# Performance work log

Hardware: AMD Instinct MI355X
Metric: run time of the kernel (lower is better)

## Reference

```python
import jax, jax.numpy as jnp
import numpy as np

N = 8192  # num_nodes
E = 8192  # num_edges (== N so self-loops sit on the diagonal)
C = 256   # in_channels
ALPHA = 0.1
BETA = 0.5


def setup_inputs() -> dict:
    key = jax.random.key(0)
    k1, k2, k3 = jax.random.split(key, 3)
    x_0 = jax.random.normal(k1, (N, C), dtype=jnp.float32)
    # binary hypergraph incidence with self-loops on the diagonal
    mask = (jax.random.uniform(k2, (N, E)) < 0.004).astype(jnp.float32)
    idx = jnp.arange(N)
    incidence_1 = mask.at[idx, idx].set(1.0)
    # torch Linear(C, C, bias=False) weight, Kaiming-uniform-ish scale
    W = jax.random.normal(k3, (C, C), dtype=jnp.float32) / jnp.sqrt(C)
    return {"x_0": x_0, "incidence_1": incidence_1, "W": W}


def reference(x_0, incidence_1, W):
    # 1) edge aggregation: m_{0->1} = B^T x  -> [E, C]
    m_0_1 = incidence_1.T @ x_0
    # degree normalization (matches diag/to_dense math without materializing diag)
    node_degree = jnp.sum(incidence_1, axis=1)                      # [N]
    edge_degree = (node_degree @ incidence_1) / jnp.sum(incidence_1, axis=0)  # [E]
    # 2) node aggregation with 1/sqrt(d_z), 1/sqrt(d_x) scaling
    m_1_0 = (incidence_1 @ (m_0_1 / jnp.sqrt(edge_degree)[:, None])) \
            / jnp.sqrt(node_degree)[:, None]                        # [N, C]
    # 3) skip + learned update (x_skip defaults to x_0)
    x_combined = (1.0 - ALPHA) * m_1_0 + ALPHA * x_0
    return (1.0 - BETA) * x_combined + BETA * (x_combined @ W.T)
```

## Files before the change

### kernel.cpp

```cpp
#include <hip/hip_runtime.h>
#include <hip/hip_bf16.h>

#define NN 8192
#define NE 8192
#define CC 256
#define CAP 128

typedef __attribute__((ext_vector_type(8))) short bf16x8;
typedef __attribute__((ext_vector_type(8))) unsigned short u16x8;
typedef __attribute__((ext_vector_type(4))) float f32x4;

static __device__ __forceinline__ ushort f2b(float f) {
    unsigned u = __float_as_uint(f);
    return (ushort)((u + 0x7fffu + ((u >> 16) & 1u)) >> 16);
}
static __device__ __forceinline__ float b2f(ushort u) {
    return __uint_as_float((unsigned)u << 16);
}

__global__ __launch_bounds__(256) void k1_scan(const float* __restrict__ B,
                                               const float* __restrict__ x0,
                                               const float* __restrict__ W,
                                               ushort* __restrict__ x0b,
                                               ushort* __restrict__ Wb,
                                               int* __restrict__ csr,
                                               int* __restrict__ row_cnt,
                                               int* __restrict__ col_cnt,
                                               int* __restrict__ csc,
                                               float* __restrict__ edge_wsum) {
    __shared__ int wcnt[4];
    {
        int i = blockIdx.x * 1024 + threadIdx.x * 4;
        float4 v = *(const float4*)(x0 + i);
        ushort4 u; u.x = f2b(v.x); u.y = f2b(v.y); u.z = f2b(v.z); u.w = f2b(v.w);
        *(ushort4*)(x0b + i) = u;
        if (blockIdx.x < 64) {
            float4 w = *(const float4*)(W + i);
            ushort4 uw; uw.x = f2b(w.x); uw.y = f2b(w.y); uw.z = f2b(w.z); uw.w = f2b(w.w);
            *(ushort4*)(Wb + i) = uw;
        }
    }
    const int wave = threadIdx.x >> 6;
    const int lane = threadIdx.x & 63;
    const int row  = blockIdx.x * 4 + wave;
    const float4* rp = (const float4*)(B + (size_t)row * NE);
    int* outp = csr + (size_t)row * CAP;
    if (lane == 0) wcnt[wave] = 0;
    float4 v = rp[lane];
    #pragma unroll 1
    for (int it = 0; it < 32; ++it) {
        float4 vn = v;
        if (it < 31) vn = rp[(it + 1) * 64 + lane];
        float fs = v.x + v.y + v.z + v.w;
        if (__ballot(fs != 0.f)) {
            int m = (int)fs;
            int pos = 0;
            if (m) pos = atomicAdd(&wcnt[wave], m);
            int e0 = (it * 64 + lane) * 4;
            if (v.x != 0.f) { if (pos < CAP) outp[pos] = e0;     ++pos; }
            if (v.y != 0.f) { if (pos < CAP) outp[pos] = e0 + 1; ++pos; }
            if (v.z != 0.f) { if (pos < CAP) outp[pos] = e0 + 2; ++pos; }
            if (v.w != 0.f) { if (pos < CAP) outp[pos] = e0 + 3; ++pos; }
        }
        v = vn;
    }
    int cnt = wcnt[wave];
    cnt = cnt < CAP ? cnt : CAP;
    if (lane == 0) row_cnt[row] = cnt;
    const float deg = (float)cnt;
    for (int i = lane; i < cnt; i += 64) {
        int e = outp[i];
        int pos = atomicAdd(&col_cnt[e], 1);
        if (pos < CAP) csc[(size_t)e * CAP + pos] = row;
        atomicAdd(&edge_wsum[e], deg);
    }
}

__global__ __launch_bounds__(256) void k4_edge_agg(const ushort* __restrict__ x0b,
                                                   const int* __restrict__ csc,
                                                   const int* __restrict__ col_cnt,
                                                   const float* __restrict__ edge_wsum,
                                                   ushort* __restrict__ m01s) {
    const int wave = threadIdx.x >> 6;
    const int lane = threadIdx.x & 63;
    const int half = lane >> 5;
    const int cl = lane & 31;
    const int e = blockIdx.x * 4 + wave;
    int cnt = col_cnt[e]; if (cnt > CAP) cnt = CAP;
    const float er = rsqrtf(edge_wsum[e] / (float)cnt);
    const int* cp = csc + (size_t)e * CAP;
    const int idx = cp[lane];
    const ushort* xb = x0b + cl * 8;
    float a0[8] = {}, a1[8] = {};
    const int lim = cnt < 64 ? cnt : 64;
    int i = 0;
    for (; i + 8 <= lim; i += 8) {
        int n0 = __shfl(idx, i + half);
        int n1 = __shfl(idx, i + 2 + half);
        int n2 = __shfl(idx, i + 4 + half);
        int n3 = __shfl(idx, i + 6 + half);
        u16x8 r0 = *(const u16x8*)(xb + (size_t)n0 * CC);
        u16x8 r1 = *(const u16x8*)(xb + (size_t)n1 * CC);
        u16x8 r2 = *(const u16x8*)(xb + (size_t)n2 * CC);
        u16x8 r3 = *(const u16x8*)(xb + (size_t)n3 * CC);
        #pragma unroll
        for (int c = 0; c < 8; ++c) {
            a0[c] += b2f(r0[c]); a1[c] += b2f(r1[c]);
            a0[c] += b2f(r2[c]); a1[c] += b2f(r3[c]);
        }
    }
    for (; i + 2 <= lim; i += 2) {
        int n0 = __shfl(idx, i + half);
        u16x8 r0 = *(const u16x8*)(xb + (size_t)n0 * CC);
        #pragma unroll
        for (int c = 0; c < 8; ++c) a0[c] += b2f(r0[c]);
    }
    if (i < lim) {
        int n0 = __shfl(idx, i);
        if (half == 0) {
            u16x8 r0 = *(const u16x8*)(xb + (size_t)n0 * CC);
            #pragma unroll
            for (int c = 0; c < 8; ++c) a0[c] += b2f(r0[c]);
        }
    }
    if (cnt > 64 && half == 0) {
        for (int j = 64; j < cnt; ++j) {
            int n2 = cp[j];
            u16x8 r0 = *(const u16x8*)(xb + (size_t)n2 * CC);
            #pragma unroll
            for (int c = 0; c < 8; ++c) a0[c] += b2f(r0[c]);
        }
    }
    u16x8 r8;
    #pragma unroll
    for (int c = 0; c < 8; ++c) {
        float t = a0[c] + a1[c];
        t += __shfl_xor(t, 32);
        r8[c] = f2b(t * er);
    }
    if (half == 0) *(u16x8*)(m01s + (size_t)e * CC + cl * 8) = r8;
}

__global__ __launch_bounds__(1024, 8) void k5_fused(const ushort* __restrict__ x0b,
                                                    const ushort* __restrict__ m01s,
                                                    const int* __restrict__ csr,
                                                    const int* __restrict__ row_cnt,
                                                    const ushort* __restrict__ Wb,
                                                    float* __restrict__ out) {
    __shared__ __align__(16) ushort xs[16][264];
    const int w = threadIdx.x >> 6;
    const int lane = threadIdx.x & 63;
    const int half = lane >> 5;
    const int cl = lane & 31;
    const int n = blockIdx.x * 16 + w;
    const int cnt = row_cnt[n];
    const float nr = rsqrtf((float)cnt);
    const int* ep = csr + (size_t)n * CAP;
    const int idx = ep[lane];
    const ushort* mb = m01s + cl * 8;
    float a0[8] = {}, a1[8] = {};
    const int lim = cnt < 64 ? cnt : 64;
    int i = 0;
    for (; i + 8 <= lim; i += 8) {
        int e0 = __shfl(idx, i + half);
        int e1 = __shfl(idx, i + 2 + half);
        int e2 = __shfl(idx, i + 4 + half);
        int e3 = __shfl(idx, i + 6 + half);
        u16x8 r0 = *(const u16x8*)(mb + (size_t)e0 * CC);
        u16x8 r1 = *(const u16x8*)(mb + (size_t)e1 * CC);
        u16x8 r2 = *(const u16x8*)(mb + (size_t)e2 * CC);
        u16x8 r3 = *(const u16x8*)(mb + (size_t)e3 * CC);
        #pragma unroll
        for (int c = 0; c < 8; ++c) {
            a0[c] += b2f(r0[c]); a1[c] += b2f(r1[c]);
            a0[c] += b2f(r2[c]); a1[c] += b2f(r3[c]);
        }
    }
    for (; i + 2 <= lim; i += 2) {
        int e0 = __shfl(idx, i + half);
        u16x8 r0 = *(const u16x8*)(mb + (size_t)e0 * CC);
        #pragma unroll
        for (int c = 0; c < 8; ++c) a0[c] += b2f(r0[c]);
    }
    if (i < lim) {
        int e0 = __shfl(idx, i);
        if (half == 0) {
            u16x8 r0 = *(const u16x8*)(mb + (size_t)e0 * CC);
            #pragma unroll
            for (int c = 0; c < 8; ++c) a0[c] += b2f(r0[c]);
        }
    }
    if (cnt > 64 && half == 0) {
        for (int j = 64; j < cnt; ++j) {
            int e2 = ep[j];
            u16x8 r0 = *(const u16x8*)(mb + (size_t)e2 * CC);
            #pragma unroll
            for (int c = 0; c < 8; ++c) a0[c] += b2f(r0[c]);
        }
    }
    u16x8 x = *(const u16x8*)(x0b + (size_t)n * CC + cl * 8);
    const float s = 0.9f * nr;
    u16x8 r8;
    #pragma unroll
    for (int c = 0; c < 8; ++c) {
        float t = a0[c] + a1[c];
        t += __shfl_xor(t, 32);
        r8[c] = f2b(s * t + 0.1f * b2f(x[c]));
    }
    if (half == 0) *(u16x8*)(&xs[w][cl * 8]) = r8;
    __syncthreads();
    const int lr = lane & 15, lk = lane >> 4;
    const int n0 = w * 16;
    f32x4 acc = {0.f, 0.f, 0.f, 0.f};
    #pragma unroll
    for (int kb = 0; kb < 8; ++kb) {
        bf16x8 a = *(const bf16x8*)(&xs[lr][kb * 32 + lk * 8]);
        bf16x8 b = *(const bf16x8*)(Wb + (size_t)(n0 + lr) * CC + kb * 32 + lk * 8);
        acc = __builtin_amdgcn_mfma_f32_16x16x32_bf16(a, b, acc, 0, 0, 0);
    }
    const size_t rb = (size_t)blockIdx.x * 16;
    #pragma unroll
    for (int r = 0; r < 4; ++r) {
        int row = lk * 4 + r;
        int col = n0 + lr;
        float sk = b2f(xs[row][col]);
        out[(rb + row) * CC + col] = 0.5f * sk + 0.5f * acc[r];
    }
}

extern "C" void kernel_launch(void* const* d_in, const int* in_sizes, int n_in,
                              void* d_out, int out_size, void* d_ws, size_t ws_size,
                              hipStream_t stream) {
    const float* x0 = (const float*)d_in[0];
    const float* B  = (const float*)d_in[1];
    const float* W  = (const float*)d_in[2];
    float* out = (float*)d_out;

    char* ws = (char*)d_ws;
    const size_t need = (17ull << 20) + 4ull * NE * 4;
    if (ws_size < need) return;

    int*    csr       = (int*)(ws);
    int*    csc       = (int*)(ws + (4ull << 20));
    ushort* m01s      = (ushort*)(ws + (8ull << 20));
    ushort* x0b       = (ushort*)(ws + (12ull << 20));
    ushort* Wb        = (ushort*)(ws + (16ull << 20));
    int*    row_cnt   = (int*)(ws + (16ull << 20) + (256u << 10));
    int*    col_cnt   = row_cnt + NN;
    float*  edge_wsum = (float*)(col_cnt + NE);

    hipMemsetAsync(col_cnt, 0, 2ull * NE * 4, stream);

    k1_scan<<<NN / 4, 256, 0, stream>>>(B, x0, W, x0b, Wb, csr, row_cnt, col_cnt, csc, edge_wsum);
    k4_edge_agg<<<NE / 4, 256, 0, stream>>>(x0b, csc, col_cnt, edge_wsum, m01s);
    k5_fused<<<NN / 16, 1024, 0, stream>>>(x0b, m01s, csr, row_cnt, Wb, out);
}
```

Before: 103.8 us.

## Split gathers into channel slabs and unfuse dense GEMM into separate kernel

The edge and node aggregation kernels now split the 256 channels into two 128-channel slabs handled by separate blocks, with four row-groups per wave gathering neighbors in parallel. This doubles the block count and changes the memory access granularity. The node kernel no longer does the W GEMM in place. It writes the combined bf16 activations to a new workspace buffer, and a new standalone MFMA GEMM kernel computes the output with four 16-column tiles per wave. This trades an extra kernel launch and a round trip of the activations through memory for better parallelism and no 1024-thread blocks with shared-memory sync.

New measurement: 111.4 us. 1.07x slower.

```diff
diff --git a/kernel.cpp b/kernel.cpp
--- a/kernel.cpp
+++ b/kernel.cpp
@@ -76,155 +76,167 @@
     }
 }
 
-__global__ __launch_bounds__(256) void k4_edge_agg(const ushort* __restrict__ x0b,
-                                                   const int* __restrict__ csc,
-                                                   const int* __restrict__ col_cnt,
-                                                   const float* __restrict__ edge_wsum,
-                                                   ushort* __restrict__ m01s) {
+__global__ __launch_bounds__(256) void k4_slab(const ushort* __restrict__ x0b,
+                                               const int* __restrict__ csc,
+                                               const int* __restrict__ col_cnt,
+                                               const float* __restrict__ edge_wsum,
+                                               ushort* __restrict__ m01s) {
     const int wave = threadIdx.x >> 6;
     const int lane = threadIdx.x & 63;
-    const int half = lane >> 5;
-    const int cl = lane & 31;
-    const int e = blockIdx.x * 4 + wave;
+    const int g = lane >> 4;
+    const int c = lane & 15;
+    const int slab = blockIdx.x & 1;
+    const int e = (blockIdx.x >> 1) * 4 + wave;
     int cnt = col_cnt[e]; if (cnt > CAP) cnt = CAP;
     const float er = rsqrtf(edge_wsum[e] / (float)cnt);
     const int* cp = csc + (size_t)e * CAP;
     const int idx = cp[lane];
-    const ushort* xb = x0b + cl * 8;
+    const ushort* xb = x0b + slab * 128 + c * 8;
     float a0[8] = {}, a1[8] = {};
     const int lim = cnt < 64 ? cnt : 64;
     int i = 0;
     for (; i + 8 <= lim; i += 8) {
-        int n0 = __shfl(idx, i + half);
-        int n1 = __shfl(idx, i + 2 + half);
-        int n2 = __shfl(idx, i + 4 + half);
-        int n3 = __shfl(idx, i + 6 + half);
-        u16x8 r0 = *(const u16x8*)(xb + (size_t)n0 * CC);
-        u16x8 r1 = *(const u16x8*)(xb + (size_t)n1 * CC);
-        u16x8 r2 = *(const u16x8*)(xb + (size_t)n2 * CC);
-        u16x8 r3 = *(const u16x8*)(xb + (size_t)n3 * CC);
-        #pragma unroll
-        for (int c = 0; c < 8; ++c) {
-            a0[c] += b2f(r0[c]); a1[c] += b2f(r1[c]);
-            a0[c] += b2f(r2[c]); a1[c] += b2f(r3[c]);
-        }
-    }
-    for (; i + 2 <= lim; i += 2) {
-        int n0 = __shfl(idx, i + half);
-        u16x8 r0 = *(const u16x8*)(xb + (size_t)n0 * CC);
-        #pragma unroll
-        for (int c = 0; c < 8; ++c) a0[c] += b2f(r0[c]);
-    }
-    if (i < lim) {
-        int n0 = __shfl(idx, i);
-        if (half == 0) {
-            u16x8 r0 = *(const u16x8*)(xb + (size_t)n0 * CC);
+        int na = __shfl(idx, i + g);
+        int nb = __shfl(idx, i + 4 + g);
+        u16x8 ra = *(const u16x8*)(xb + (size_t)na * CC);
+        u16x8 rb = *(const u16x8*)(xb + (size_t)nb * CC);
+        #pragma unroll
+        for (int k = 0; k < 8; ++k) { a0[k] += b2f(ra[k]); a1[k] += b2f(rb[k]); }
+    }
+    if (i + 4 <= lim) {
+        int na = __shfl(idx, i + g);
+        u16x8 ra = *(const u16x8*)(xb + (size_t)na * CC);
+        #pragma unroll
+        for (int k = 0; k < 8; ++k) a0[k] += b2f(ra[k]);
+        i += 4;
+    }
+    {
+        int na = __shfl(idx, (i + g) & 63);
+        if (i + g < lim) {
+            u16x8 ra = *(const u16x8*)(xb + (size_t)na * CC);
             #pragma unroll
-            for (int c = 0; c < 8; ++c) a0[c] += b2f(r0[c]);
-        }
-    }
-    if (cnt > 64 && half == 0) {
+            for (int k = 0; k < 8; ++k) a0[k] += b2f(ra[k]);
+        }
+    }
+    if (cnt > 64) {
         for (int j = 64; j < cnt; ++j) {
             int n2 = cp[j];
-            u16x8 r0 = *(const u16x8*)(xb + (size_t)n2 * CC);
-            #pragma unroll
-            for (int c = 0; c < 8; ++c) a0[c] += b2f(r0[c]);
+            if (g == 0) {
+                u16x8 ra = *(const u16x8*)(xb + (size_t)n2 * CC);
+                #pragma unroll
+                for (int k = 0; k < 8; ++k) a0[k] += b2f(ra[k]);
+            }
         }
     }
     u16x8 r8;
     #pragma unroll
-    for (int c = 0; c < 8; ++c) {
-        float t = a0[c] + a1[c];
+    for (int k = 0; k < 8; ++k) {
+        float t = a0[k] + a1[k];
+        t += __shfl_xor(t, 16);
         t += __shfl_xor(t, 32);
-        r8[c] = f2b(t * er);
-    }
-    if (half == 0) *(u16x8*)(m01s + (size_t)e * CC + cl * 8) = r8;
-}
-
-__global__ __launch_bounds__(1024, 8) void k5_fused(const ushort* __restrict__ x0b,
-                                                    const ushort* __restrict__ m01s,
-                                                    const int* __restrict__ csr,
-                                                    const int* __restrict__ row_cnt,
-                                                    const ushort* __restrict__ Wb,
-                                                    float* __restrict__ out) {
-    __shared__ __align__(16) ushort xs[16][264];
-    const int w = threadIdx.x >> 6;
-    const int lane = threadIdx.x & 63;
-    const int half = lane >> 5;
-    const int cl = lane & 31;
-    const int n = blockIdx.x * 16 + w;
+        r8[k] = f2b(t * er);
+    }
+    if (g == 0) *(u16x8*)(m01s + (size_t)e * CC + slab * 128 + c * 8) = r8;
+}
+
+__global__ __launch_bounds__(256) void k5_slab(const ushort* __restrict__ x0b,
+                                               const ushort* __restrict__ m01s,
+                                               const int* __restrict__ csr,
+                                               const int* __restrict__ row_cnt,
+                                               ushort* __restrict__ xcb) {
+    const int wave = threadIdx.x >> 6;
+    const int lane = threadIdx.x & 63;
+    const int g = lane >> 4;
+    const int c = lane & 15;
+    const int slab = blockIdx.x & 1;
+    const int n = (blockIdx.x >> 1) * 4 + wave;
     const int cnt = row_cnt[n];
     const float nr = rsqrtf((float)cnt);
     const int* ep = csr + (size_t)n * CAP;
     const int idx = ep[lane];
-    const ushort* mb = m01s + cl * 8;
+    const ushort* mb = m01s + slab * 128 + c * 8;
     float a0[8] = {}, a1[8] = {};
     const int lim = cnt < 64 ? cnt : 64;
     int i = 0;
     for (; i + 8 <= lim; i += 8) {
-        int e0 = __shfl(idx, i + half);
-        int e1 = __shfl(idx, i + 2 + half);
-        int e2 = __shfl(idx, i + 4 + half);
-        int e3 = __shfl(idx, i + 6 + half);
-        u16x8 r0 = *(const u16x8*)(mb + (size_t)e0 * CC);
-        u16x8 r1 = *(const u16x8*)(mb + (size_t)e1 * CC);
-        u16x8 r2 = *(const u16x8*)(mb + (size_t)e2 * CC);
-        u16x8 r3 = *(const u16x8*)(mb + (size_t)e3 * CC);
-        #pragma unroll
-        for (int c = 0; c < 8; ++c) {
-            a0[c] += b2f(r0[c]); a1[c] += b2f(r1[c]);
-            a0[c] += b2f(r2[c]); a1[c] += b2f(r3[c]);
-        }
-    }
-    for (; i + 2 <= lim; i += 2) {
-        int e0 = __shfl(idx, i + half);
-        u16x8 r0 = *(const u16x8*)(mb + (size_t)e0 * CC);
-        #pragma unroll
-        for (int c = 0; c < 8; ++c) a0[c] += b2f(r0[c]);
-    }
-    if (i < lim) {
-        int e0 = __shfl(idx, i);
-        if (half == 0) {
-            u16x8 r0 = *(const u16x8*)(mb + (size_t)e0 * CC);
+        int ea = __shfl(idx, i + g);
+        int eb = __shfl(idx, i + 4 + g);
+        u16x8 ra = *(const u16x8*)(mb + (size_t)ea * CC);
+        u16x8 rb = *(const u16x8*)(mb + (size_t)eb * CC);
+        #pragma unroll
+        for (int k = 0; k < 8; ++k) { a0[k] += b2f(ra[k]); a1[k] += b2f(rb[k]); }
+    }
+    if (i + 4 <= lim) {
+        int ea = __shfl(idx, i + g);
+        u16x8 ra = *(const u16x8*)(mb + (size_t)ea * CC);
+        #pragma unroll
+        for (int k = 0; k < 8; ++k) a0[k] += b2f(ra[k]);
+        i += 4;
+    }
+    {
+        int ea = __shfl(idx, (i + g) & 63);
+        if (i + g < lim) {
+            u16x8 ra = *(const u16x8*)(mb + (size_t)ea * CC);
             #pragma unroll
-            for (int c = 0; c < 8; ++c) a0[c] += b2f(r0[c]);
-        }
-    }
-    if (cnt > 64 && half == 0) {
+            for (int k = 0; k < 8; ++k) a0[k] += b2f(ra[k]);
+        }
+    }
+    if (cnt > 64) {
         for (int j = 64; j < cnt; ++j) {
             int e2 = ep[j];
-            u16x8 r0 = *(const u16x8*)(mb + (size_t)e2 * CC);
-            #pragma unroll
-            for (int c = 0; c < 8; ++c) a0[c] += b2f(r0[c]);
-        }
-    }
-    u16x8 x = *(const u16x8*)(x0b + (size_t)n * CC + cl * 8);
-    const float s = 0.9f * nr;
-    u16x8 r8;
-    #pragma unroll
-    for (int c = 0; c < 8; ++c) {
-        float t = a0[c] + a1[c];
-        t += __shfl_xor(t, 32);
-        r8[c] = f2b(s * t + 0.1f * b2f(x[c]));
-    }
-    if (half == 0) *(u16x8*)(&xs[w][cl * 8]) = r8;
-    __syncthreads();
+            if (g == 0) {
+                u16x8 ra = *(const u16x8*)(mb + (size_t)e2 * CC);
+                #pragma unroll
+                for (int k = 0; k < 8; ++k) a0[k] += b2f(ra[k]);
+            }
+        }
+    }
+    float t[8];
+    #pragma unroll
+    for (int k = 0; k < 8; ++k) {
+        float s = a0[k] + a1[k];
+        s += __shfl_xor(s, 16);
+        s += __shfl_xor(s, 32);
+        t[k] = s;
+    }
+    if (g == 0) {
+        u16x8 x = *(const u16x8*)(x0b + (size_t)n * CC + slab * 128 + c * 8);
+        const float s = 0.9f * nr;
+        u16x8 r8;
+        #pragma unroll
+        for (int k = 0; k < 8; ++k) r8[k] = f2b(s * t[k] + 0.1f * b2f(x[k]));
+        *(u16x8*)(xcb + (size_t)n * CC + slab * 128 + c * 8) = r8;
+    }
+}
+
+__global__ __launch_bounds__(256) void k6_gemm(const ushort* __restrict__ xcb,
+                                               const ushort* __restrict__ Wb,
+                                               float* __restrict__ out) {
+    const int lane = threadIdx.x & 63;
+    const int gw = blockIdx.x * 4 + (threadIdx.x >> 6);
+    const int m0 = (gw >> 2) * 16;
+    const int n0 = (gw & 3) * 64;
     const int lr = lane & 15, lk = lane >> 4;
-    const int n0 = w * 16;
-    f32x4 acc = {0.f, 0.f, 0.f, 0.f};
+    f32x4 acc[4] = {};
+    const ushort* ap = xcb + (size_t)(m0 + lr) * CC + lk * 8;
     #pragma unroll
     for (int kb = 0; kb < 8; ++kb) {
-        bf16x8 a = *(const bf16x8*)(&xs[lr][kb * 32 + lk * 8]);
-        bf16x8 b = *(const bf16x8*)(Wb + (size_t)(n0 + lr) * CC + kb * 32 + lk * 8);
-        acc = __builtin_amdgcn_mfma_f32_16x16x32_bf16(a, b, acc, 0, 0, 0);
-    }
-    const size_t rb = (size_t)blockIdx.x * 16;
-    #pragma unroll
-    for (int r = 0; r < 4; ++r) {
-        int row = lk * 4 + r;
-        int col = n0 + lr;
-        float sk = b2f(xs[row][col]);
-        out[(rb + row) * CC + col] = 0.5f * sk + 0.5f * acc[r];
+        bf16x8 a = *(const bf16x8*)(ap + kb * 32);
+        #pragma unroll
+        for (int j = 0; j < 4; ++j) {
+            bf16x8 b = *(const bf16x8*)(Wb + (size_t)(n0 + j * 16 + lr) * CC + kb * 32 + lk * 8);
+            acc[j] = __builtin_amdgcn_mfma_f32_16x16x32_bf16(a, b, acc[j], 0, 0, 0);
+        }
+    }
+    #pragma unroll
+    for (int j = 0; j < 4; ++j) {
+        #pragma unroll
+        for (int r = 0; r < 4; ++r) {
+            int row = m0 + lk * 4 + r;
+            int col = n0 + j * 16 + lr;
+            float sk = b2f(xcb[(size_t)row * CC + col]);
+            out[(size_t)row * CC + col] = 0.5f * sk + 0.5f * acc[j][r];
+        }
     }
 }
 
@@ -237,21 +249,23 @@
     float* out = (float*)d_out;
 
     char* ws = (char*)d_ws;
-    const size_t need = (17ull << 20) + 4ull * NE * 4;
+    const size_t need = (21ull << 20) + 4ull * NE * 4;
     if (ws_size < need) return;
 
     int*    csr       = (int*)(ws);
     int*    csc       = (int*)(ws + (4ull << 20));
     ushort* m01s      = (ushort*)(ws + (8ull << 20));
-    ushort* x0b       = (ushort*)(ws + (12ull << 20));
-    ushort* Wb        = (ushort*)(ws + (16ull << 20));
-    int*    row_cnt   = (int*)(ws + (16ull << 20) + (256u << 10));
+    ushort* xcb       = (ushort*)(ws + (12ull << 20));
+    ushort* x0b       = (ushort*)(ws + (16ull << 20));
+    ushort* Wb        = (ushort*)(ws + (20ull << 20));
+    int*    row_cnt   = (int*)(ws + (20ull << 20) + (256u << 10));
     int*    col_cnt   = row_cnt + NN;
     float*  edge_wsum = (float*)(col_cnt + NE);
 
     hipMemsetAsync(col_cnt, 0, 2ull * NE * 4, stream);
 
     k1_scan<<<NN / 4, 256, 0, stream>>>(B, x0, W, x0b, Wb, csr, row_cnt, col_cnt, csc, edge_wsum);
-    k4_edge_agg<<<NE / 4, 256, 0, stream>>>(x0b, csc, col_cnt, edge_wsum, m01s);
-    k5_fused<<<NN / 16, 1024, 0, stream>>>(x0b, m01s, csr, row_cnt, Wb, out);
-}
+    k4_slab<<<NE / 4 * 2, 256, 0, stream>>>(x0b, csc, col_cnt, edge_wsum, m01s);
+    k5_slab<<<NN / 4 * 2, 256, 0, stream>>>(x0b, m01s, csr, row_cnt, xcb);
+    k6_gemm<<<NN * CC / 16 / 64 / 4, 256, 0, stream>>>(xcb, Wb, out);
+}
```

## Fuse scan, edge aggregation and node update into one cooperative persistent kernel

Applied to the files above, without the earlier changes.

Replaces the memset and three separate launches with one cooperative kernel of 256 blocks of 1024 threads, using grid-wide syncs between the phases: CSR scan, CSC/atomic build, edge aggregation, and node aggregation plus MFMA. The col_cnt/edge_wsum zeroing moves inside the kernel and the scan phase loses its software prefetch. The aim is to remove launch gaps and the memset. In exchange, each block covers 32 rows per phase with only 256 blocks and one block per CU, which lowers occupancy for the bandwidth-bound scan of the 256 MB incidence matrix and adds the cost of the grid syncs.

Result: slower. 211.4 us (+103.7%).

```diff
diff --git a/kernel.cpp b/kernel.cpp
--- a/kernel.cpp
+++ b/kernel.cpp
@@ -1,10 +1,15 @@
 #include <hip/hip_runtime.h>
+#include <hip/hip_cooperative_groups.h>
 #include <hip/hip_bf16.h>
+
+namespace cg = cooperative_groups;
 
 #define NN 8192
 #define NE 8192
 #define CC 256
 #define CAP 128
+#define NB 256
+#define NTH 1024
 
 typedef __attribute__((ext_vector_type(8))) short bf16x8;
 typedef __attribute__((ext_vector_type(8))) unsigned short u16x8;
@@ -18,213 +23,222 @@
     return __uint_as_float((unsigned)u << 16);
 }
 
-__global__ __launch_bounds__(256) void k1_scan(const float* __restrict__ B,
-                                               const float* __restrict__ x0,
-                                               const float* __restrict__ W,
-                                               ushort* __restrict__ x0b,
-                                               ushort* __restrict__ Wb,
-                                               int* __restrict__ csr,
-                                               int* __restrict__ row_cnt,
-                                               int* __restrict__ col_cnt,
-                                               int* __restrict__ csc,
-                                               float* __restrict__ edge_wsum) {
-    __shared__ int wcnt[4];
+__global__ __launch_bounds__(NTH, 1) void fused_all(
+        const float* __restrict__ B, const float* __restrict__ x0,
+        const float* __restrict__ W,
+        ushort* __restrict__ x0b, ushort* __restrict__ Wb,
+        int* __restrict__ csr, int* __restrict__ row_cnt,
+        int* __restrict__ col_cnt, int* __restrict__ csc,
+        float* __restrict__ edge_wsum, ushort* __restrict__ m01s,
+        float* __restrict__ out) {
+    cg::grid_group grid = cg::this_grid();
+    const int tid  = threadIdx.x;
+    const int bid  = blockIdx.x;
+    const int w    = tid >> 6;
+    const int lane = tid & 63;
+    const int half = lane >> 5;
+    const int cl   = lane & 31;
+    __shared__ int wcnt[16];
+    __shared__ __align__(16) ushort xs[32][264];
+
     {
-        int i = blockIdx.x * 1024 + threadIdx.x * 4;
-        float4 v = *(const float4*)(x0 + i);
-        ushort4 u; u.x = f2b(v.x); u.y = f2b(v.y); u.z = f2b(v.z); u.w = f2b(v.w);
-        *(ushort4*)(x0b + i) = u;
-        if (blockIdx.x < 64) {
-            float4 w = *(const float4*)(W + i);
-            ushort4 uw; uw.x = f2b(w.x); uw.y = f2b(w.y); uw.z = f2b(w.z); uw.w = f2b(w.w);
-            *(ushort4*)(Wb + i) = uw;
-        }
-    }
-    const int wave = threadIdx.x >> 6;
-    const int lane = threadIdx.x & 63;
-    const int row  = blockIdx.x * 4 + wave;
-    const float4* rp = (const float4*)(B + (size_t)row * NE);
-    int* outp = csr + (size_t)row * CAP;
-    if (lane == 0) wcnt[wave] = 0;
-    float4 v = rp[lane];
-    #pragma unroll 1
-    for (int it = 0; it < 32; ++it) {
-        float4 vn = v;
-        if (it < 31) vn = rp[(it + 1) * 64 + lane];
-        float fs = v.x + v.y + v.z + v.w;
-        if (__ballot(fs != 0.f)) {
-            int m = (int)fs;
-            int pos = 0;
-            if (m) pos = atomicAdd(&wcnt[wave], m);
-            int e0 = (it * 64 + lane) * 4;
-            if (v.x != 0.f) { if (pos < CAP) outp[pos] = e0;     ++pos; }
-            if (v.y != 0.f) { if (pos < CAP) outp[pos] = e0 + 1; ++pos; }
-            if (v.z != 0.f) { if (pos < CAP) outp[pos] = e0 + 2; ++pos; }
-            if (v.w != 0.f) { if (pos < CAP) outp[pos] = e0 + 3; ++pos; }
-        }
-        v = vn;
-    }
-    int cnt = wcnt[wave];
-    cnt = cnt < CAP ? cnt : CAP;
-    if (lane == 0) row_cnt[row] = cnt;
-    const float deg = (float)cnt;
-    for (int i = lane; i < cnt; i += 64) {
-        int e = outp[i];
-        int pos = atomicAdd(&col_cnt[e], 1);
-        if (pos < CAP) csc[(size_t)e * CAP + pos] = row;
-        atomicAdd(&edge_wsum[e], deg);
-    }
-}
-
-__global__ __launch_bounds__(256) void k4_edge_agg(const ushort* __restrict__ x0b,
-                                                   const int* __restrict__ csc,
-                                                   const int* __restrict__ col_cnt,
-                                                   const float* __restrict__ edge_wsum,
-                                                   ushort* __restrict__ m01s) {
-    const int wave = threadIdx.x >> 6;
-    const int lane = threadIdx.x & 63;
-    const int half = lane >> 5;
-    const int cl = lane & 31;
-    const int e = blockIdx.x * 4 + wave;
-    int cnt = col_cnt[e]; if (cnt > CAP) cnt = CAP;
-    const float er = rsqrtf(edge_wsum[e] / (float)cnt);
-    const int* cp = csc + (size_t)e * CAP;
-    const int idx = cp[lane];
-    const ushort* xb = x0b + cl * 8;
-    float a0[8] = {}, a1[8] = {};
-    const int lim = cnt < 64 ? cnt : 64;
-    int i = 0;
-    for (; i + 8 <= lim; i += 8) {
-        int n0 = __shfl(idx, i + half);
-        int n1 = __shfl(idx, i + 2 + half);
-        int n2 = __shfl(idx, i + 4 + half);
-        int n3 = __shfl(idx, i + 6 + half);
-        u16x8 r0 = *(const u16x8*)(xb + (size_t)n0 * CC);
-        u16x8 r1 = *(const u16x8*)(xb + (size_t)n1 * CC);
-        u16x8 r2 = *(const u16x8*)(xb + (size_t)n2 * CC);
-        u16x8 r3 = *(const u16x8*)(xb + (size_t)n3 * CC);
+        int z = bid * NTH + tid;
+        if (z < 2 * NE) col_cnt[z] = 0;
+        int i = (bid * NTH + tid) * 8;
+        f32x4 v0 = *(const f32x4*)(x0 + i);
+        f32x4 v1 = *(const f32x4*)(x0 + i + 4);
+        u16x8 u;
+        u[0]=f2b(v0.x); u[1]=f2b(v0.y); u[2]=f2b(v0.z); u[3]=f2b(v0.w);
+        u[4]=f2b(v1.x); u[5]=f2b(v1.y); u[6]=f2b(v1.z); u[7]=f2b(v1.w);
+        *(u16x8*)(x0b + i) = u;
+        if (bid < 8) {
+            f32x4 w0 = *(const f32x4*)(W + i);
+            f32x4 w1 = *(const f32x4*)(W + i + 4);
+            u16x8 uw;
+            uw[0]=f2b(w0.x); uw[1]=f2b(w0.y); uw[2]=f2b(w0.z); uw[3]=f2b(w0.w);
+            uw[4]=f2b(w1.x); uw[5]=f2b(w1.y); uw[6]=f2b(w1.z); uw[7]=f2b(w1.w);
+            *(u16x8*)(Wb + i) = uw;
+        }
+    }
+    int cnts[2];
+    #pragma unroll 1
+    for (int rr = 0; rr < 2; ++rr) {
+        const int row = bid * 32 + w * 2 + rr;
+        const f32x4* rp = (const f32x4*)(B + (size_t)row * NE);
+        int* outp = csr + (size_t)row * CAP;
+        if (lane == 0) wcnt[w] = 0;
+        #pragma unroll 1
+        for (int it = 0; it < 32; ++it) {
+            f32x4 v = rp[it * 64 + lane];
+            float fs = v.x + v.y + v.z + v.w;
+            if (__ballot(fs != 0.f)) {
+                int m = (int)fs;
+                int pos = 0;
+                if (m) pos = atomicAdd(&wcnt[w], m);
+                int e0 = (it * 64 + lane) * 4;
+                if (v.x != 0.f) { if (pos < CAP) outp[pos] = e0;     ++pos; }
+                if (v.y != 0.f) { if (pos < CAP) outp[pos] = e0 + 1; ++pos; }
+                if (v.z != 0.f) { if (pos < CAP) outp[pos] = e0 + 2; ++pos; }
+                if (v.w != 0.f) { if (pos < CAP) outp[pos] = e0 + 3; ++pos; }
+            }
+        }
+        int c = wcnt[w];
+        c = c < CAP ? c : CAP;
+        cnts[rr] = c;
+        if (lane == 0) row_cnt[row] = c;
+    }
+    grid.sync();
+    #pragma unroll 1
+    for (int rr = 0; rr < 2; ++rr) {
+        const int row = bid * 32 + w * 2 + rr;
+        const int cnt = cnts[rr];
+        const float deg = (float)cnt;
+        const int* outp = csr + (size_t)row * CAP;
+        for (int i = lane; i < cnt; i += 64) {
+            int e = outp[i];
+            int pos = atomicAdd(&col_cnt[e], 1);
+            if (pos < CAP) csc[(size_t)e * CAP + pos] = row;
+            atomicAdd(&edge_wsum[e], deg);
+        }
+    }
+    grid.sync();
+    #pragma unroll 1
+    for (int ee = 0; ee < 2; ++ee) {
+        const int e = bid * 32 + ee * 16 + w;
+        int cnt = col_cnt[e]; if (cnt > CAP) cnt = CAP;
+        const float er = rsqrtf(edge_wsum[e] / (float)cnt);
+        const int* cp = csc + (size_t)e * CAP;
+        const int idx = cp[lane];
+        const ushort* xb = x0b + cl * 8;
+        float a0[8] = {}, a1[8] = {};
+        const int lim = cnt < 64 ? cnt : 64;
+        int i = 0;
+        for (; i + 8 <= lim; i += 8) {
+            int n0 = __shfl(idx, i + half);
+            int n1 = __shfl(idx, i + 2 + half);
+            int n2 = __shfl(idx, i + 4 + half);
+            int n3 = __shfl(idx, i + 6 + half);
+            u16x8 r0 = *(const u16x8*)(xb + (size_t)n0 * CC);
+            u16x8 r1 = *(const u16x8*)(xb + (size_t)n1 * CC);
+            u16x8 r2 = *(const u16x8*)(xb + (size_t)n2 * CC);
+            u16x8 r3 = *(const u16x8*)(xb + (size_t)n3 * CC);
+            #pragma unroll
+            for (int c = 0; c < 8; ++c) {
+                a0[c] += b2f(r0[c]); a1[c] += b2f(r1[c]);
+                a0[c] += b2f(r2[c]); a1[c] += b2f(r3[c]);
+            }
+        }
+        for (; i + 2 <= lim; i += 2) {
+            int n0 = __shfl(idx, i + half);
+            u16x8 r0 = *(const u16x8*)(xb + (size_t)n0 * CC);
+            #pragma unroll
+            for (int c = 0; c < 8; ++c) a0[c] += b2f(r0[c]);
+        }
+        if (i < lim) {
+            int n0 = __shfl(idx, i);
+            if (half == 0) {
+                u16x8 r0 = *(const u16x8*)(xb + (size_t)n0 * CC);
+                #pragma unroll
+                for (int c = 0; c < 8; ++c) a0[c] += b2f(r0[c]);
+            }
+        }
+        if (cnt > 64 && half == 0) {
+            for (int j = 64; j < cnt; ++j) {
+                int n2 = cp[j];
+                u16x8 r0 = *(const u16x8*)(xb + (size_t)n2 * CC);
+                #pragma unroll
+                for (int c = 0; c < 8; ++c) a0[c] += b2f(r0[c]);
+            }
+        }
+        u16x8 r8;
         #pragma unroll
         for (int c = 0; c < 8; ++c) {
-            a0[c] += b2f(r0[c]); a1[c] += b2f(r1[c]);
-            a0[c] += b2f(r2[c]); a1[c] += b2f(r3[c]);
-        }
-    }
-    for (; i + 2 <= lim; i += 2) {
-        int n0 = __shfl(idx, i + half);
-        u16x8 r0 = *(const u16x8*)(xb + (size_t)n0 * CC);
-        #pragma unroll
-        for (int c = 0; c < 8; ++c) a0[c] += b2f(r0[c]);
-    }
-    if (i < lim) {
-        int n0 = __shfl(idx, i);
-        if (half == 0) {
-            u16x8 r0 = *(const u16x8*)(xb + (size_t)n0 * CC);
+            float t = a0[c] + a1[c];
+            t += __shfl_xor(t, 32);
+            r8[c] = f2b(t * er);
+        }
+        if (half == 0) *(u16x8*)(m01s + (size_t)e * CC + cl * 8) = r8;
+    }
+    grid.sync();
+    #pragma unroll 1
+    for (int nn2 = 0; nn2 < 2; ++nn2) {
+        const int n = bid * 32 + nn2 * 16 + w;
+        const int cnt = row_cnt[n];
+        const float nr = rsqrtf((float)cnt);
+        const int* ep = csr + (size_t)n * CAP;
+        const int idx = ep[lane];
+        const ushort* mb = m01s + cl * 8;
+        float a0[8] = {}, a1[8] = {};
+        const int lim = cnt < 64 ? cnt : 64;
+        int i = 0;
+        for (; i + 8 <= lim; i += 8) {
+            int e0 = __shfl(idx, i + half);
+            int e1 = __shfl(idx, i + 2 + half);
+            int e2 = __shfl(idx, i + 4 + half);
+            int e3 = __shfl(idx, i + 6 + half);
+            u16x8 r0 = *(const u16x8*)(mb + (size_t)e0 * CC);
+            u16x8 r1 = *(const u16x8*)(mb + (size_t)e1 * CC);
+            u16x8 r2 = *(const u16x8*)(mb + (size_t)e2 * CC);
+            u16x8 r3 = *(const u16x8*)(mb + (size_t)e3 * CC);
+            #pragma unroll
+            for (int c = 0; c < 8; ++c) {
+                a0[c] += b2f(r0[c]); a1[c] += b2f(r1[c]);
+                a0[c] += b2f(r2[c]); a1[c] += b2f(r3[c]);
+            }
+        }
+        for (; i + 2 <= lim; i += 2) {
+            int e0 = __shfl(idx, i + half);
+            u16x8 r0 = *(const u16x8*)(mb + (size_t)e0 * CC);
             #pragma unroll
             for (int c = 0; c < 8; ++c) a0[c] += b2f(r0[c]);
         }
-    }
-    if (cnt > 64 && half == 0) {
-        for (int j = 64; j < cnt; ++j) {
-            int n2 = cp[j];
-            u16x8 r0 = *(const u16x8*)(xb + (size_t)n2 * CC);
-            #pragma unroll
-            for (int c = 0; c < 8; ++c) a0[c] += b2f(r0[c]);
-        }
-    }
-    u16x8 r8;
-    #pragma unroll
-    for (int c = 0; c < 8; ++c) {
-        float t = a0[c] + a1[c];
-        t += __shfl_xor(t, 32);
-        r8[c] = f2b(t * er);
-    }
-    if (half == 0) *(u16x8*)(m01s + (size_t)e * CC + cl * 8) = r8;
-}
-
-__global__ __launch_bounds__(1024, 8) void k5_fused(const ushort* __restrict__ x0b,
-                                                    const ushort* __restrict__ m01s,
-                                                    const int* __restrict__ csr,
-                                                    const int* __restrict__ row_cnt,
-                                                    const ushort* __restrict__ Wb,
-                                                    float* __restrict__ out) {
-    __shared__ __align__(16) ushort xs[16][264];
-    const int w = threadIdx.x >> 6;
-    const int lane = threadIdx.x & 63;
-    const int half = lane >> 5;
-    const int cl = lane & 31;
-    const int n = blockIdx.x * 16 + w;
-    const int cnt = row_cnt[n];
-    const float nr = rsqrtf((float)cnt);
-    const int* ep = csr + (size_t)n * CAP;
-    const int idx = ep[lane];
-    const ushort* mb = m01s + cl * 8;
-    float a0[8] = {}, a1[8] = {};
-    const int lim = cnt < 64 ? cnt : 64;
-    int i = 0;
-    for (; i + 8 <= lim; i += 8) {
-        int e0 = __shfl(idx, i + half);
-        int e1 = __shfl(idx, i + 2 + half);
-        int e2 = __shfl(idx, i + 4 + half);
-        int e3 = __shfl(idx, i + 6 + half);
-        u16x8 r0 = *(const u16x8*)(mb + (size_t)e0 * CC);
-        u16x8 r1 = *(const u16x8*)(mb + (size_t)e1 * CC);
-        u16x8 r2 = *(const u16x8*)(mb + (size_t)e2 * CC);
-        u16x8 r3 = *(const u16x8*)(mb + (size_t)e3 * CC);
+        if (i < lim) {
+            int e0 = __shfl(idx, i);
+            if (half == 0) {
+                u16x8 r0 = *(const u16x8*)(mb + (size_t)e0 * CC);
+                #pragma unroll
+                for (int c = 0; c < 8; ++c) a0[c] += b2f(r0[c]);
+            }
+        }
+        if (cnt > 64 && half == 0) {
+            for (int j = 64; j < cnt; ++j) {
+                int e2 = ep[j];
+                u16x8 r0 = *(const u16x8*)(mb + (size_t)e2 * CC);
+                #pragma unroll
+                for (int c = 0; c < 8; ++c) a0[c] += b2f(r0[c]);
+            }
+        }
+        u16x8 x = *(const u16x8*)(x0b + (size_t)n * CC + cl * 8);
+        const float s = 0.9f * nr;
+        u16x8 r8;
         #pragma unroll
         for (int c = 0; c < 8; ++c) {
-            a0[c] += b2f(r0[c]); a1[c] += b2f(r1[c]);
-            a0[c] += b2f(r2[c]); a1[c] += b2f(r3[c]);
-        }
-    }
-    for (; i + 2 <= lim; i += 2) {
-        int e0 = __shfl(idx, i + half);
-        u16x8 r0 = *(const u16x8*)(mb + (size_t)e0 * CC);
+            float t = a0[c] + a1[c];
+            t += __shfl_xor(t, 32);
+            r8[c] = f2b(s * t + 0.1f * b2f(x[c]));
+        }
+        if (half == 0) *(u16x8*)(&xs[nn2 * 16 + w][cl * 8]) = r8;
+    }
+    __syncthreads();
+    {
+        const int lr = lane & 15, lk = lane >> 4;
+        const int col = w * 16 + lr;
         #pragma unroll
-        for (int c = 0; c < 8; ++c) a0[c] += b2f(r0[c]);
-    }
-    if (i < lim) {
-        int e0 = __shfl(idx, i);
-        if (half == 0) {
-            u16x8 r0 = *(const u16x8*)(mb + (size_t)e0 * CC);
-            #pragma unroll
-            for (int c = 0; c < 8; ++c) a0[c] += b2f(r0[c]);
-        }
-    }
-    if (cnt > 64 && half == 0) {
-        for (int j = 64; j < cnt; ++j) {
-            int e2 = ep[j];
-            u16x8 r0 = *(const u16x8*)(mb + (size_t)e2 * CC);
-            #pragma unroll
-            for (int c = 0; c < 8; ++c) a0[c] += b2f(r0[c]);
-        }
-    }
-    u16x8 x = *(const u16x8*)(x0b + (size_t)n * CC + cl * 8);
-    const float s = 0.9f * nr;
-    u16x8 r8;
-    #pragma unroll
-    for (int c = 0; c < 8; ++c) {
-        float t = a0[c] + a1[c];
-        t += __shfl_xor(t, 32);
-        r8[c] = f2b(s * t + 0.1f * b2f(x[c]));
-    }
-    if (half == 0) *(u16x8*)(&xs[w][cl * 8]) = r8;
-    __syncthreads();
-    const int lr = lane & 15, lk = lane >> 4;
-    const int n0 = w * 16;
-    f32x4 acc = {0.f, 0.f, 0.f, 0.f};
-    #pragma unroll
-    for (int kb = 0; kb < 8; ++kb) {
-        bf16x8 a = *(const bf16x8*)(&xs[lr][kb * 32 + lk * 8]);
-        bf16x8 b = *(const bf16x8*)(Wb + (size_t)(n0 + lr) * CC + kb * 32 + lk * 8);
-        acc = __builtin_amdgcn_mfma_f32_16x16x32_bf16(a, b, acc, 0, 0, 0);
-    }
-    const size_t rb = (size_t)blockIdx.x * 16;
-    #pragma unroll
-    for (int r = 0; r < 4; ++r) {
-        int row = lk * 4 + r;
-        int col = n0 + lr;
-        float sk = b2f(xs[row][col]);
-        out[(rb + row) * CC + col] = 0.5f * sk + 0.5f * acc[r];
+        for (int rt = 0; rt < 2; ++rt) {
+            f32x4 acc = {0.f, 0.f, 0.f, 0.f};
+            #pragma unroll
+            for (int kb = 0; kb < 8; ++kb) {
+                bf16x8 a = *(const bf16x8*)(&xs[rt * 16 + lr][kb * 32 + lk * 8]);
+                bf16x8 b = *(const bf16x8*)(Wb + (size_t)(w * 16 + lr) * CC + kb * 32 + lk * 8);
+                acc = __builtin_amdgcn_mfma_f32_16x16x32_bf16(a, b, acc, 0, 0, 0);
+            }
+            #pragma unroll
+            for (int r = 0; r < 4; ++r) {
+                int row = rt * 16 + lk * 4 + r;
+                float sk = b2f(xs[row][col]);
+                out[(size_t)(bid * 32 + row) * CC + col] = 0.5f * sk + 0.5f * acc[r];
+            }
+        }
     }
 }
 
@@ -237,7 +251,7 @@
     float* out = (float*)d_out;
 
     char* ws = (char*)d_ws;
-    const size_t need = (17ull << 20) + 4ull * NE * 4;
+    const size_t need = (16ull << 20) + (512ull << 10);
     if (ws_size < need) return;
 
     int*    csr       = (int*)(ws);
@@ -249,9 +263,12 @@
     int*    col_cnt   = row_cnt + NN;
     float*  edge_wsum = (float*)(col_cnt + NE);
 
-    hipMemsetAsync(col_cnt, 0, 2ull * NE * 4, stream);
-
-    k1_scan<<<NN / 4, 256, 0, stream>>>(B, x0, W, x0b, Wb, csr, row_cnt, col_cnt, csc, edge_wsum);
-    k4_edge_agg<<<NE / 4, 256, 0, stream>>>(x0b, csc, col_cnt, edge_wsum, m01s);
-    k5_fused<<<NN / 16, 1024, 0, stream>>>(x0b, m01s, csr, row_cnt, Wb, out);
-}
+    void* args[] = {
+        (void*)&B, (void*)&x0, (void*)&W,
+        (void*)&x0b, (void*)&Wb,
+        (void*)&csr, (void*)&row_cnt, (void*)&col_cnt, (void*)&csc,
+        (void*)&edge_wsum, (void*)&m01s, (void*)&out
+    };
+    hipLaunchCooperativeKernel((const void*)fused_all, dim3(NB), dim3(NTH),
+                               args, 0, stream);
+}
```
